# Kernel optimization log

Measured on AMD Instinct MI355X. Metric: run time of the kernel, lower is better.

Reference implementation:

```python
import jax, jax.numpy as jnp
import numpy as np

# fp4 e2m1 representable magnitudes and rounding midpoints
FP4_LEVELS = jnp.array([0.0, 0.5, 1.0, 1.5, 2.0, 3.0, 4.0, 6.0], dtype=jnp.float32)
FP4_BOUNDS = jnp.array([0.25, 0.75, 1.25, 1.75, 2.5, 3.5, 5.0], dtype=jnp.float32)
EPS = 1e-8
RANK = 64      # activation_lowrank_svd
NITER = 2      # activation_lowrank_niter


def fp4_get_scalar(x):
    # per-tensor scale: amax / max_fp4e2m1 (6.0)
    return jnp.maximum(jnp.max(jnp.abs(x)) / 6.0, EPS)


def fp4_qdq(x):
    # quant (round-to-nearest fp4e2m1 grid) followed by rquant (dequant)
    s = fp4_get_scalar(x)
    y = x / s
    a = jnp.clip(jnp.abs(y), 0.0, 6.0)
    idx = jnp.searchsorted(FP4_BOUNDS, a)  # nearest-level index
    return jnp.sign(y) * FP4_LEVELS[idx] * s


def power_iter_svd(G, V0, niter):
    # Dion-style power iteration: G ~ U diag(S) V^T, V0: [n,k]
    V = V0
    U = None
    W = None
    for it in range(niter):
        P = G @ V                                  # [m,k]
        U, _ = jnp.linalg.qr(P)                    # reduced QR, U: [m,k]
        W = G.T @ U                                # [n,k]
        if it < niter - 1:
            V = W / (jnp.linalg.norm(W, axis=0, keepdims=True) + EPS)
    S = jnp.linalg.norm(W, axis=0)                 # [k]
    Vn = W / (S[None, :] + EPS)                    # [n,k]
    return U, S, Vn


def svd_quant(x2d, V0):
    # low-rank kernel + fp4-quantized factors + fp4-quantized residual
    U, S, V = power_iter_svd(x2d, V0, NITER)
    ug = U.T                                       # [k,m]
    vg = V.T                                       # [k,n]
    ker = (U * S[None, :]) @ vg                    # [m,n] full-precision kernel
    ugq = fp4_qdq(ug)
    vgq = fp4_qdq(vg)
    res_q = fp4_qdq(x2d - ker)                     # quantized residual
    return (ugq.T * S[None, :]) @ vgq + res_q      # reconstructed input


def setup_inputs() -> dict:
    key = jax.random.key(0)
    k1, k2, k3, k4 = jax.random.split(key, 4)
    B, Sq, Din, Dout, R = 4, 2048, 4096, 4096, RANK
    x = jax.random.normal(k1, (B, Sq, Din), jnp.float32)
    weight = jax.random.normal(k2, (Dout, Din), jnp.float32) * (1.0 / np.sqrt(Din))
    bias = jax.random.normal(k3, (Dout,), jnp.float32) * 0.01
    V0 = jax.random.normal(k4, (Din, R), jnp.float32)  # cached subspace (state)
    return {"x": x, "weight": weight, "bias": bias, "V0": V0}


def reference(x, weight, bias, V0):
    B, Sq, Din = x.shape
    # activation SVD + fp4 quantization on flattened [B*S, Din]
    xq = svd_quant(x.reshape(-1, Din), V0).reshape(B, Sq, Din)
    # weight fp4 quant/dequant
    wq = fp4_qdq(weight)
    return xq @ wq.T + bias
```

## Files before the change

### kernel.cpp

```cpp
#include <hip/hip_runtime.h>
#include <stdint.h>

#define EPSF 1e-8f
#define KT 4160

typedef float  f32x4  __attribute__((ext_vector_type(4)));
typedef __bf16 bf16x8 __attribute__((ext_vector_type(8)));
typedef __bf16 bf16x4 __attribute__((ext_vector_type(4)));

constexpr size_t oP    = 0;
constexpr size_t oW    = oP  + 8192*64;
constexpr size_t oG    = oW  + 4096*64;
constexpr size_t oM1   = oG  + 64*64;
constexpr size_t oScal = oM1 + 64*4096;
constexpr size_t nZero1= oScal + 4;
constexpr size_t nZero2= oG + 64*64;
constexpr size_t oS    = nZero1;
constexpr size_t oLinv = oS + 64;
constexpr size_t oV    = oLinv + 64*64;
constexpr size_t oU    = oV + 4096*64;
constexpr size_t endF32= oU + 8192*64;
constexpr size_t bfByte= ((endF32*4 + 255)/256)*256;
constexpr size_t oVq   = 0;
constexpr size_t oA    = oVq + 64*4096;
constexpr size_t oB    = oA + (size_t)8192*4160;
constexpr size_t oVcT  = oB + (size_t)4096*4160;
constexpr size_t oUT   = oVcT + 3*(size_t)64*4096;
constexpr size_t oUhl  = oUT + 3*(size_t)64*8192;
constexpr size_t oKVT  = oUhl + 2*(size_t)8192*64;
constexpr size_t endBF = oKVT + 2*(size_t)4096*64;
constexpr size_t WS_NEED = bfByte + endBF*2;

__device__ __forceinline__ float qlevel(float a){
  if (a <= 0.25f) return 0.0f;
  if (a <= 0.75f) return 0.5f;
  if (a <= 1.25f) return 1.0f;
  if (a <= 1.75f) return 1.5f;
  if (a <= 2.5f)  return 2.0f;
  if (a <= 3.5f)  return 3.0f;
  if (a <= 5.0f)  return 4.0f;
  return 6.0f;
}
__device__ __forceinline__ float qgrid(float v, float s){
  float y = v / s;
  float l = qlevel(fabsf(y));
  return y < 0.0f ? -l : l;
}

__global__ void k_zero(float* p, int n){
  for (int i = blockIdx.x*blockDim.x + threadIdx.x; i < n; i += gridDim.x*blockDim.x)
    p[i] = 0.0f;
}

__global__ void k_amax4(const float4* __restrict__ x, int n4, unsigned* __restrict__ out){
  float m = 0.f;
  for (int i = blockIdx.x*blockDim.x + threadIdx.x; i < n4; i += gridDim.x*blockDim.x){
    float4 v = x[i];
    m = fmaxf(m, fmaxf(fmaxf(fabsf(v.x), fabsf(v.y)), fmaxf(fabsf(v.z), fabsf(v.w))));
  }
  for (int o = 32; o > 0; o >>= 1) m = fmaxf(m, __shfl_down(m, o, 64));
  __shared__ float sm[4];
  int lane = threadIdx.x & 63, w = threadIdx.x >> 6;
  if (lane == 0) sm[w] = m;
  __syncthreads();
  if (threadIdx.x == 0)
    atomicMax(out, __float_as_uint(fmaxf(fmaxf(sm[0],sm[1]), fmaxf(sm[2],sm[3]))));
}

__global__ __launch_bounds__(256) void k_gv(
    float* __restrict__ P, const float* __restrict__ x,
    const __bf16* __restrict__ Bh, const __bf16* __restrict__ Bm, const __bf16* __restrict__ Bl){
  int m0 = blockIdx.x * 128;
  int d0 = blockIdx.y * 512;
  int lane = threadIdx.x & 63, wave = threadIdx.x >> 6;
  int kgrp = lane >> 4, lrow = lane & 15;
  f32x4 acc[2][4] = {};
  for (int dc = d0; dc < d0 + 512; dc += 32){
    bf16x8 ah[2], am[2], al[2];
    #pragma unroll
    for (int f = 0; f < 2; f++){
      const float* g = x + (size_t)(m0 + wave*32 + f*16 + lrow)*4096 + dc + kgrp*8;
      float4 a = *(const float4*)g;
      float4 b = *(const float4*)(g + 4);
      float v[8] = {a.x,a.y,a.z,a.w,b.x,b.y,b.z,b.w};
      #pragma unroll
      for (int j = 0; j < 8; j++){
        __bf16 h = (__bf16)v[j];
        float r1 = v[j] - (float)h;
        __bf16 md = (__bf16)r1;
        float r2 = r1 - (float)md;
        ah[f][j] = h; am[f][j] = md; al[f][j] = (__bf16)r2;
      }
    }
    #pragma unroll
    for (int n = 0; n < 4; n++){
      size_t bo = (size_t)(n*16 + lrow)*4096 + dc + kgrp*8;
      bf16x8 bh = *(const bf16x8*)(Bh + bo);
      bf16x8 bm = *(const bf16x8*)(Bm + bo);
      bf16x8 bl = *(const bf16x8*)(Bl + bo);
      #pragma unroll
      for (int f = 0; f < 2; f++){
        acc[f][n] = __builtin_amdgcn_mfma_f32_16x16x32_bf16(ah[f], bh, acc[f][n],0,0,0);
        acc[f][n] = __builtin_amdgcn_mfma_f32_16x16x32_bf16(ah[f], bm, acc[f][n],0,0,0);
        acc[f][n] = __builtin_amdgcn_mfma_f32_16x16x32_bf16(am[f], bh, acc[f][n],0,0,0);
        acc[f][n] = __builtin_amdgcn_mfma_f32_16x16x32_bf16(ah[f], bl, acc[f][n],0,0,0);
        acc[f][n] = __builtin_amdgcn_mfma_f32_16x16x32_bf16(al[f], bh, acc[f][n],0,0,0);
        acc[f][n] = __builtin_amdgcn_mfma_f32_16x16x32_bf16(am[f], bm, acc[f][n],0,0,0);
      }
    }
  }
  #pragma unroll
  for (int f = 0; f < 2; f++)
    #pragma unroll
    for (int n = 0; n < 4; n++)
      #pragma unroll
      for (int r = 0; r < 4; r++)
        atomicAdd(&P[(size_t)(m0 + wave*32 + f*16 + kgrp*4 + r)*64 + n*16 + lrow], acc[f][n][r]);
}

__global__ __launch_bounds__(256) void k_gtu(
    float* __restrict__ W, const float* __restrict__ x,
    const __bf16* __restrict__ Bh, const __bf16* __restrict__ Bm, const __bf16* __restrict__ Bl){
  int d0 = blockIdx.x * 64;
  int m0 = blockIdx.y * 1024;
  int lane = threadIdx.x & 63, wave = threadIdx.x >> 6;
  int kgrp = lane >> 4, lrow = lane & 15;
  int dcol = d0 + wave*16 + lrow;
  f32x4 acc[4] = {};
  for (int mc = m0; mc < m0 + 1024; mc += 32){
    bf16x8 ah, am, al;
    int mb = mc + kgrp*8;
    #pragma unroll
    for (int j = 0; j < 8; j++){
      float v = x[(size_t)(mb + j)*4096 + dcol];
      __bf16 h = (__bf16)v;
      float r1 = v - (float)h;
      __bf16 md = (__bf16)r1;
      float r2 = r1 - (float)md;
      ah[j] = h; am[j] = md; al[j] = (__bf16)r2;
    }
    #pragma unroll
    for (int n = 0; n < 4; n++){
      size_t bo = (size_t)(n*16 + lrow)*8192 + mc + kgrp*8;
      bf16x8 bh = *(const bf16x8*)(Bh + bo);
      bf16x8 bm = *(const bf16x8*)(Bm + bo);
      bf16x8 bl = *(const bf16x8*)(Bl + bo);
      acc[n] = __builtin_amdgcn_mfma_f32_16x16x32_bf16(ah, bh, acc[n],0,0,0);
      acc[n] = __builtin_amdgcn_mfma_f32_16x16x32_bf16(ah, bm, acc[n],0,0,0);
      acc[n] = __builtin_amdgcn_mfma_f32_16x16x32_bf16(am, bh, acc[n],0,0,0);
      acc[n] = __builtin_amdgcn_mfma_f32_16x16x32_bf16(ah, bl, acc[n],0,0,0);
      acc[n] = __builtin_amdgcn_mfma_f32_16x16x32_bf16(al, bh, acc[n],0,0,0);
      acc[n] = __builtin_amdgcn_mfma_f32_16x16x32_bf16(am, bm, acc[n],0,0,0);
    }
  }
  #pragma unroll
  for (int n = 0; n < 4; n++)
    #pragma unroll
    for (int r = 0; r < 4; r++)
      atomicAdd(&W[(size_t)(d0 + wave*16 + kgrp*4 + r)*64 + n*16 + lrow], acc[n][r]);
}

__global__ void k_gram(const float* __restrict__ P, float* __restrict__ Gram){
  __shared__ float Pt[128][65];
  int m0 = blockIdx.x * 128;
  int t = threadIdx.x;
  for (int i = 0; i < 32; i++){
    int idx = i*256 + t; int r = idx >> 6, c = idx & 63;
    Pt[r][c] = P[(size_t)(m0+r)*64 + c];
  }
  __syncthreads();
  int ti = t >> 4, tj = t & 15;
  float acc[4][4] = {};
  for (int r = 0; r < 128; r++){
    float a[4], b[4];
    #pragma unroll
    for (int q = 0; q < 4; q++) a[q] = Pt[r][ti*4+q];
    #pragma unroll
    for (int q = 0; q < 4; q++) b[q] = Pt[r][tj*4+q];
    #pragma unroll
    for (int xx = 0; xx < 4; xx++)
      #pragma unroll
      for (int y = 0; y < 4; y++) acc[xx][y] += a[xx]*b[y];
  }
  for (int xx = 0; xx < 4; xx++)
    for (int y = 0; y < 4; y++)
      atomicAdd(&Gram[(ti*4+xx)*64 + tj*4+y], acc[xx][y]);
}

__global__ void k_cholinv(const float* __restrict__ Gram, float* __restrict__ Linv){
  __shared__ double A[64][64];
  __shared__ double Li[64][64];
  int t = threadIdx.x;
  for (int j = 0; j < 64; j++){ A[t][j] = (double)Gram[t*64+j]; Li[t][j] = 0.0; }
  __syncthreads();
  for (int k = 0; k < 64; k++){
    if (t == k) A[k][k] = sqrt(A[k][k]);
    __syncthreads();
    if (t > k) A[t][k] /= A[k][k];
    __syncthreads();
    if (t > k){
      double aik = A[t][k];
      for (int j = k+1; j <= t; j++) A[t][j] -= aik * A[j][k];
    }
    __syncthreads();
  }
  for (int i = t; i < 64; i++){
    double s = (i == t) ? 1.0 : 0.0;
    for (int p = t; p < i; p++) s -= A[i][p] * Li[p][t];
    Li[i][t] = s / A[i][i];
  }
  __syncthreads();
  for (int j = 0; j < 64; j++) Linv[t*64+j] = (float)Li[t][j];
}

__global__ void k_applyq(float* __restrict__ U, const float* __restrict__ P,
                         const float* __restrict__ Linv){
  __shared__ float Pt[64][65];
  __shared__ float Lt[64][65];
  int m0 = blockIdx.x * 64;
  int t = threadIdx.x;
  for (int i = 0; i < 16; i++){
    int idx = i*256 + t; int r = idx >> 6, c = idx & 63;
    Pt[r][c] = P[(size_t)(m0+r)*64 + c];
    Lt[r][c] = Linv[r*64 + c];
  }
  __syncthreads();
  int tm = t >> 4, tj = t & 15;
  float acc[4][4] = {};
  for (int i = 0; i < 64; i++){
    float p[4], lv[4];
    #pragma unroll
    for (int a = 0; a < 4; a++) p[a]  = Pt[tm*4+a][i];
    #pragma unroll
    for (int b = 0; b < 4; b++) lv[b] = Lt[tj*4+b][i];
    #pragma unroll
    for (int a = 0; a < 4; a++)
      #pragma unroll
      for (int b = 0; b < 4; b++) acc[a][b] += p[a]*lv[b];
  }
  for (int a = 0; a < 4; a++)
    for (int b = 0; b < 4; b++)
      U[(size_t)(m0+tm*4+a)*64 + tj*4+b] = acc[a][b];
}

__global__ void k_colnorm(const float* __restrict__ W, float* __restrict__ cn){
  int k = blockIdx.x;
  float s = 0.f;
  for (int d = threadIdx.x; d < 4096; d += 256){
    float v = W[(size_t)d*64 + k];
    s += v*v;
  }
  for (int o = 32; o > 0; o >>= 1) s += __shfl_down(s, o, 64);
  __shared__ float sm[4];
  int lane = threadIdx.x & 63, w = threadIdx.x >> 6;
  if (lane == 0) sm[w] = s;
  __syncthreads();
  if (threadIdx.x == 0) cn[k] = sqrtf(sm[0]+sm[1]+sm[2]+sm[3]);
}

__global__ void k_vnorm(float* __restrict__ V, const float* __restrict__ W,
                        const float* __restrict__ cn){
  int i = blockIdx.x*256 + threadIdx.x;
  int k = i & 63;
  V[i] = W[i] / (cn[k] + EPSF);
}

__global__ void k_vnkv(float* __restrict__ V, __bf16* __restrict__ Kh, __bf16* __restrict__ Kl,
                       const float* __restrict__ W, const float* __restrict__ S,
                       unsigned* __restrict__ amaxv){
  int i = blockIdx.x*256 + threadIdx.x;
  int k = i & 63, d = i >> 6;
  float s = S[k];
  float vn = W[i] / (s + EPSF);
  V[i] = vn;
  float kv = s * vn;
  __bf16 h = (__bf16)kv;
  Kh[(size_t)d*64 + k] = h;
  Kl[(size_t)d*64 + k] = (__bf16)(kv - (float)h);
  float m = fabsf(vn);
  for (int o = 32; o > 0; o >>= 1) m = fmaxf(m, __shfl_down(m, o, 64));
  __shared__ float sm[4];
  int lane = threadIdx.x & 63, w = threadIdx.x >> 6;
  if (lane == 0) sm[w] = m;
  __syncthreads();
  if (threadIdx.x == 0)
    atomicMax(amaxv, __float_as_uint(fmaxf(fmaxf(sm[0],sm[1]), fmaxf(sm[2],sm[3]))));
}

__global__ void k_prep_vct(const float* __restrict__ Vc, __bf16* __restrict__ Th,
                           __bf16* __restrict__ Tm, __bf16* __restrict__ Tl){
  __shared__ float Vt[64][65];
  int d0 = blockIdx.x * 64;
  int t = threadIdx.x;
  for (int i = 0; i < 16; i++){
    int idx = i*256 + t; int r = idx >> 6, c = idx & 63;
    Vt[r][c] = Vc[(size_t)(d0 + r)*64 + c];
  }
  __syncthreads();
  for (int i = 0; i < 16; i++){
    int idx = i*256 + t; int k = idx >> 6, dd = idx & 63;
    float v = Vt[dd][k];
    __bf16 h = (__bf16)v;
    float r1 = v - (float)h;
    __bf16 md = (__bf16)r1;
    float r2 = r1 - (float)md;
    size_t o = (size_t)k*4096 + d0 + dd;
    Th[o] = h; Tm[o] = md; Tl[o] = (__bf16)r2;
  }
}

__global__ void k_prep_u(const float* __restrict__ Ub, __bf16* __restrict__ Uh, __bf16* __restrict__ Ul,
                         __bf16* __restrict__ Th, __bf16* __restrict__ Tm, __bf16* __restrict__ Tl){
  __shared__ float Ut[64][65];
  int m0 = blockIdx.x * 64;
  int t = threadIdx.x;
  for (int i = 0; i < 16; i++){
    int idx = i*256 + t; int r = idx >> 6, c = idx & 63;
    float v = Ub[(size_t)(m0 + r)*64 + c];
    Ut[r][c] = v;
    __bf16 h = (__bf16)v;
    Uh[(size_t)(m0+r)*64 + c] = h;
    Ul[(size_t)(m0+r)*64 + c] = (__bf16)(v - (float)h);
  }
  __syncthreads();
  for (int i = 0; i < 16; i++){
    int idx = i*256 + t; int k = idx >> 6, mm = idx & 63;
    float v = Ut[mm][k];
    __bf16 h = (__bf16)v;
    float r1 = v - (float)h;
    __bf16 md = (__bf16)r1;
    float r2 = r1 - (float)md;
    size_t o = (size_t)k*8192 + m0 + mm;
    Th[o] = h; Tm[o] = md; Tl[o] = (__bf16)r2;
  }
}

__global__ void k_qw(__bf16* __restrict__ Bq, const float* __restrict__ w,
                     const unsigned* __restrict__ amaxw){
  float s = fmaxf(__uint_as_float(*amaxw) / 6.0f, EPSF);
  int i = blockIdx.x*256 + threadIdx.x;
  int n = i >> 10, d = (i & 1023)*4;
  float4 v = *(const float4*)(w + (size_t)n*4096 + d);
  bf16x4 o;
  o[0] = (__bf16)qgrid(v.x, s); o[1] = (__bf16)qgrid(v.y, s);
  o[2] = (__bf16)qgrid(v.z, s); o[3] = (__bf16)qgrid(v.w, s);
  *(bf16x4*)(Bq + (size_t)n*4160 + d) = o;
}

__global__ void k_qu(__bf16* __restrict__ Aq, const float* __restrict__ U,
                     const unsigned* __restrict__ amaxu){
  float s = fmaxf(__uint_as_float(*amaxu) / 6.0f, EPSF);
  int i = blockIdx.x*256 + threadIdx.x;
  int m = i >> 6, k = i & 63;
  Aq[(size_t)m*4160 + 4096 + k] = (__bf16)qgrid(U[i], s);
}

__global__ void k_qv(__bf16* __restrict__ Vq, const float* __restrict__ V,
                     const unsigned* __restrict__ amaxv){
  __shared__ float Vt[64][65];
  float s = fmaxf(__uint_as_float(*amaxv)/6.0f, EPSF);
  int d0 = blockIdx.x * 64;
  int t = threadIdx.x;
  for (int i = 0; i < 16; i++){
    int idx = i*256 + t; int r = idx >> 6, c = idx & 63;
    Vt[r][c] = V[(size_t)(d0 + r)*64 + c];
  }
  __syncthreads();
  for (int i = 0; i < 16; i++){
    int idx = i*256 + t; int k = idx >> 6, dd = idx & 63;
    Vq[(size_t)k*4096 + d0 + dd] = (__bf16)qgrid(Vt[dd][k], s);
  }
}

__global__ __launch_bounds__(256) void k_res(
    const float* __restrict__ x, const __bf16* __restrict__ Uh, const __bf16* __restrict__ Ul,
    const __bf16* __restrict__ Kh, const __bf16* __restrict__ Kl,
    unsigned* __restrict__ amaxr, __bf16* __restrict__ Aq, int mode){
  int m0 = blockIdx.x * 64, n0 = blockIdx.y * 128;
  int lane = threadIdx.x & 63, wave = threadIdx.x >> 6;
  int kgrp = lane >> 4, lrow = lane & 15;
  int mrow = m0 + wave*16 + lrow;
  f32x4 acc[8] = {};
  #pragma unroll
  for (int ks = 0; ks < 2; ks++){
    size_t ao = (size_t)mrow*64 + ks*32 + kgrp*8;
    bf16x8 uh = *(const bf16x8*)(Uh + ao);
    bf16x8 ul = *(const bf16x8*)(Ul + ao);
    #pragma unroll
    for (int n = 0; n < 8; n++){
      size_t bo = (size_t)(n0 + n*16 + lrow)*64 + ks*32 + kgrp*8;
      bf16x8 kh = *(const bf16x8*)(Kh + bo);
      bf16x8 kl = *(const bf16x8*)(Kl + bo);
      acc[n] = __builtin_amdgcn_mfma_f32_16x16x32_bf16(uh, kh, acc[n],0,0,0);
      acc[n] = __builtin_amdgcn_mfma_f32_16x16x32_bf16(uh, kl, acc[n],0,0,0);
      acc[n] = __builtin_amdgcn_mfma_f32_16x16x32_bf16(ul, kh, acc[n],0,0,0);
    }
  }
  int mb = m0 + wave*16 + kgrp*4;
  if (mode == 0){
    float mx = 0.f;
    #pragma unroll
    for (int n = 0; n < 8; n++){
      int c = n0 + n*16 + lrow;
      #pragma unroll
      for (int r = 0; r < 4; r++)
        mx = fmaxf(mx, fabsf(x[(size_t)(mb + r)*4096 + c] - acc[n][r]));
    }
    for (int o = 32; o > 0; o >>= 1) mx = fmaxf(mx, __shfl_down(mx, o, 64));
    __shared__ float sm[4];
    if (lane == 0) sm[wave] = mx;
    __syncthreads();
    if (threadIdx.x == 0)
      atomicMax(amaxr, __float_as_uint(fmaxf(fmaxf(sm[0],sm[1]), fmaxf(sm[2],sm[3]))));
  } else {
    float s = fmaxf(__uint_as_float(*amaxr)/6.0f, EPSF);
    #pragma unroll
    for (int n = 0; n < 8; n++){
      int c = n0 + n*16 + lrow;
      #pragma unroll
      for (int r = 0; r < 4; r++)
        Aq[(size_t)(mb + r)*4160 + c] =
          (__bf16)qgrid(x[(size_t)(mb + r)*4096 + c] - acc[n][r], s);
    }
  }
}

__global__ __launch_bounds__(256) void k_m1(
    float* __restrict__ M1g, const __bf16* __restrict__ Vq, const __bf16* __restrict__ Bq){
  int n0 = blockIdx.x * 64;
  int k0 = blockIdx.y * 512;
  int lane = threadIdx.x & 63, wave = threadIdx.x >> 6;
  int kgrp = lane >> 4, lrow = lane & 15;
  int nrow = n0 + wave*16 + lrow;
  f32x4 acc[4] = {};
  for (int kc = k0; kc < k0 + 512; kc += 32){
    bf16x8 fb = *(const bf16x8*)(Bq + (size_t)nrow*4160 + kc + kgrp*8);
    #pragma unroll
    for (int mt = 0; mt < 4; mt++){
      bf16x8 fa = *(const bf16x8*)(Vq + (size_t)(mt*16 + lrow)*4096 + kc + kgrp*8);
      acc[mt] = __builtin_amdgcn_mfma_f32_16x16x32_bf16(fa, fb, acc[mt],0,0,0);
    }
  }
  #pragma unroll
  for (int mt = 0; mt < 4; mt++)
    #pragma unroll
    for (int r = 0; r < 4; r++)
      atomicAdd(&M1g[(size_t)(mt*16 + kgrp*4 + r)*4096 + nrow], acc[mt][r]);
}

__global__ void k_m2t(__bf16* __restrict__ Bq, const float* __restrict__ M1g,
                      const float* __restrict__ S, const unsigned* __restrict__ scal){
  float su = fmaxf(__uint_as_float(scal[1])/6.0f, EPSF);
  float sv = fmaxf(__uint_as_float(scal[2])/6.0f, EPSF);
  float sr = fmaxf(__uint_as_float(scal[3])/6.0f, EPSF);
  int i = blockIdx.x*256 + threadIdx.x;
  int n = i >> 6, k = i & 63;
  float v = M1g[(size_t)k*4096 + n] * (su * sv * S[k] / sr);
  Bq[(size_t)n*4160 + 4096 + k] = (__bf16)v;
}

__global__ __launch_bounds__(256)
void k_gemm(float* __restrict__ out, const __bf16* __restrict__ A,
            const __bf16* __restrict__ B, const float* __restrict__ bias,
            const unsigned* __restrict__ scal){
  __shared__ __align__(16) __bf16 As[128*64];
  __shared__ __align__(16) __bf16 Bs[128*64];
  int m0 = blockIdx.y * 128, n0 = blockIdx.x * 128;
  int t = threadIdx.x;
  int lane = t & 63;
  int wave = t >> 6;
  int wrow = wave & 1, wcol = wave >> 1;
  f32x4 acc[4][4] = {};

  for (int kt = 0; kt < KT; kt += 64){
    #pragma unroll
    for (int i = 0; i < 4; i++){
      int idx = i*256 + t;
      int r = idx >> 3, slot = idx & 7;
      int c = slot ^ (r & 7);
      const __bf16* ga = A + (size_t)(m0 + r)*KT + kt + c*8;
      const __bf16* gb = B + (size_t)(n0 + r)*KT + kt + c*8;
      __bf16* la = As + (size_t)(i*256 + (t & ~63))*8;
      __bf16* lb = Bs + (size_t)(i*256 + (t & ~63))*8;
      __builtin_amdgcn_global_load_lds((const __attribute__((address_space(1))) uint32_t*)ga,
                                       (__attribute__((address_space(3))) uint32_t*)la, 16, 0, 0);
      __builtin_amdgcn_global_load_lds((const __attribute__((address_space(1))) uint32_t*)gb,
                                       (__attribute__((address_space(3))) uint32_t*)lb, 16, 0, 0);
    }
    __syncthreads();
    #pragma unroll
    for (int ks = 0; ks < 2; ks++){
      bf16x8 fa[4], fb[4];
      int c = ks*4 + (lane >> 4);
      #pragma unroll
      for (int f = 0; f < 4; f++){
        int row = wrow*64 + f*16 + (lane & 15);
        fa[f] = *(const bf16x8*)(As + ((size_t)row*8 + (c ^ (row & 7)))*8);
        int col = wcol*64 + f*16 + (lane & 15);
        fb[f] = *(const bf16x8*)(Bs + ((size_t)col*8 + (c ^ (col & 7)))*8);
      }
      #pragma unroll
      for (int fm = 0; fm < 4; fm++)
        #pragma unroll
        for (int fn = 0; fn < 4; fn++)
          acc[fm][fn] = __builtin_amdgcn_mfma_f32_16x16x32_bf16(fa[fm], fb[fn], acc[fm][fn], 0, 0, 0);
    }
    __syncthreads();
  }

  float sr = fmaxf(__uint_as_float(scal[3])/6.0f, EPSF);
  float sw = fmaxf(__uint_as_float(scal[0])/6.0f, EPSF);
  float srw = sr * sw;
  #pragma unroll
  for (int fn = 0; fn < 4; fn++){
    int n = n0 + wcol*64 + fn*16 + (lane & 15);
    float bs = bias[n];
    #pragma unroll
    for (int fm = 0; fm < 4; fm++){
      int mb = m0 + wrow*64 + fm*16 + 4*(lane >> 4);
      #pragma unroll
      for (int r = 0; r < 4; r++)
        out[(size_t)(mb + r)*4096 + n] = acc[fm][fn][r] * srw + bs;
    }
  }
}

extern "C" void kernel_launch(void* const* d_in, const int* in_sizes, int n_in,
                              void* d_out, int out_size, void* d_ws, size_t ws_size,
                              hipStream_t stream){
  const float* x    = (const float*)d_in[0];
  const float* wt   = (const float*)d_in[1];
  const float* bias = (const float*)d_in[2];
  const float* V0   = (const float*)d_in[3];
  float* out = (float*)d_out;
  if (ws_size < WS_NEED) return;

  float* F = (float*)d_ws;
  unsigned* scal = (unsigned*)(F + oScal);
  __bf16* BFp = (__bf16*)((char*)d_ws + bfByte);
  __bf16* Vq  = BFp + oVq;
  __bf16* Aq  = BFp + oA;
  __bf16* Bq  = BFp + oB;
  __bf16* VcTh = BFp + oVcT,              *VcTm = VcTh + (size_t)64*4096, *VcTl = VcTm + (size_t)64*4096;
  __bf16* UTh  = BFp + oUT,               *UTm  = UTh + (size_t)64*8192,  *UTl  = UTm + (size_t)64*8192;
  __bf16* Uh   = BFp + oUhl,              *Ul   = Uh + (size_t)8192*64;
  __bf16* KVTh = BFp + oKVT,              *KVTl = KVTh + (size_t)4096*64;
  float *P = F+oP, *W = F+oW, *Gm = F+oG, *M1 = F+oM1, *Sv = F+oS,
        *Li = F+oLinv, *V = F+oV, *Ub = F+oU;

  dim3 b256(256);
  k_zero <<<dim3(2048), b256, 0, stream>>>(F, (int)nZero1);
  k_amax4<<<dim3(1024), b256, 0, stream>>>((const float4*)wt, 4194304, scal+0);
  k_qw   <<<dim3(16384), b256, 0, stream>>>(Bq, wt, scal+0);

  k_prep_vct<<<dim3(64),  b256, 0, stream>>>(V0, VcTh, VcTm, VcTl);
  k_gv     <<<dim3(64,8), b256, 0, stream>>>(P, x, VcTh, VcTm, VcTl);
  k_gram   <<<dim3(64),   b256, 0, stream>>>(P, Gm);
  k_cholinv<<<dim3(1), dim3(64), 0, stream>>>(Gm, Li);
  k_applyq <<<dim3(128),  b256, 0, stream>>>(Ub, P, Li);
  k_prep_u <<<dim3(128),  b256, 0, stream>>>(Ub, Uh, Ul, UTh, UTm, UTl);
  k_gtu    <<<dim3(64,8), b256, 0, stream>>>(W, x, UTh, UTm, UTl);
  k_colnorm<<<dim3(64),   b256, 0, stream>>>(W, Sv);
  k_vnorm  <<<dim3(1024), b256, 0, stream>>>(V, W, Sv);

  k_prep_vct<<<dim3(64),  b256, 0, stream>>>(V, VcTh, VcTm, VcTl);
  k_zero   <<<dim3(2048), b256, 0, stream>>>(F, (int)nZero2);
  k_gv     <<<dim3(64,8), b256, 0, stream>>>(P, x, VcTh, VcTm, VcTl);
  k_gram   <<<dim3(64),   b256, 0, stream>>>(P, Gm);
  k_cholinv<<<dim3(1), dim3(64), 0, stream>>>(Gm, Li);
  k_applyq <<<dim3(128),  b256, 0, stream>>>(Ub, P, Li);
  k_prep_u <<<dim3(128),  b256, 0, stream>>>(Ub, Uh, Ul, UTh, UTm, UTl);
  k_gtu    <<<dim3(64,8), b256, 0, stream>>>(W, x, UTh, UTm, UTl);
  k_colnorm<<<dim3(64),   b256, 0, stream>>>(W, Sv);
  k_vnkv   <<<dim3(1024), b256, 0, stream>>>(V, KVTh, KVTl, W, Sv, scal+2);

  k_amax4<<<dim3(1024), b256, 0, stream>>>((const float4*)Ub, 131072, scal+1);
  k_qu   <<<dim3(2048), b256, 0, stream>>>(Aq, Ub, scal+1);
  k_qv   <<<dim3(64),   b256, 0, stream>>>(Vq, V, scal+2);
  k_res  <<<dim3(128,32), b256, 0, stream>>>(x, Uh, Ul, KVTh, KVTl, scal+3, Aq, 0);
  k_res  <<<dim3(128,32), b256, 0, stream>>>(x, Uh, Ul, KVTh, KVTl, scal+3, Aq, 1);

  k_m1  <<<dim3(64,8), b256, 0, stream>>>(M1, Vq, Bq);
  k_m2t <<<dim3(1024), b256, 0, stream>>>(Bq, M1, Sv, scal);
  k_gemm<<<dim3(32,64), b256, 0, stream>>>(out, Aq, Bq, bias, scal);
}
```

Baseline: 1.634 ms.

## Enlarge GEMM tiles to 256x256 with 4-stage async LDS pipeline

Reworks the final bf16 GEMM from 128x128 tiles with 256 threads and a synchronous load/compute loop into 256x256 tiles with 512 threads. A 4-deep ring of 32-wide K slices in LDS is filled by direct global-to-LDS loads issued three steps ahead, and partial vmcnt waits with a single barrier per step replace the two syncthreads. MFMA issue priority is raised with setprio. The aim is to hide global load latency and raise arithmetic intensity per block, at the cost of 128 KB of LDS, more accumulator registers, and fewer blocks (512).

```diff
diff --git a/kernel.cpp b/kernel.cpp
--- a/kernel.cpp
+++ b/kernel.cpp
@@ -459,68 +459,97 @@
   Bq[(size_t)n*4160 + 4096 + k] = (__bf16)v;
 }
 
-__global__ __launch_bounds__(256)
+__global__ __launch_bounds__(512, 2)
 void k_gemm(float* __restrict__ out, const __bf16* __restrict__ A,
             const __bf16* __restrict__ B, const float* __restrict__ bias,
             const unsigned* __restrict__ scal){
-  __shared__ __align__(16) __bf16 As[128*64];
-  __shared__ __align__(16) __bf16 Bs[128*64];
-  int m0 = blockIdx.y * 128, n0 = blockIdx.x * 128;
-  int t = threadIdx.x;
-  int lane = t & 63;
-  int wave = t >> 6;
-  int wrow = wave & 1, wcol = wave >> 1;
-  f32x4 acc[4][4] = {};
-
-  for (int kt = 0; kt < KT; kt += 64){
-    #pragma unroll
-    for (int i = 0; i < 4; i++){
-      int idx = i*256 + t;
-      int r = idx >> 3, slot = idx & 7;
-      int c = slot ^ (r & 7);
-      const __bf16* ga = A + (size_t)(m0 + r)*KT + kt + c*8;
-      const __bf16* gb = B + (size_t)(n0 + r)*KT + kt + c*8;
-      __bf16* la = As + (size_t)(i*256 + (t & ~63))*8;
-      __bf16* lb = Bs + (size_t)(i*256 + (t & ~63))*8;
+  __shared__ __align__(16) __bf16 As[4*8192];
+  __shared__ __align__(16) __bf16 Bs[4*8192];
+  const int m0 = blockIdx.y * 256, n0 = blockIdx.x * 256;
+  const int tid = threadIdx.x;
+  const int lane = tid & 63, wave = tid >> 6;
+  const int wrow = wave >> 2, wcol = wave & 3;
+  const int kg = lane >> 4, lr = lane & 15;
+  f32x4 acc[8][4] = {};
+
+  auto STAGE = [&](int tt){
+    __bf16* as = &As[(tt & 3) * 8192];
+    __bf16* bs = &Bs[(tt & 3) * 8192];
+    const int kt = tt * 32;
+    #pragma unroll
+    for (int q = 0; q < 2; q++){
+      int idx = q * 512 + tid;
+      int rp  = idx >> 3;
+      int sp  = (idx & 7) ^ (rp & 7);
+      int grow = rp * 2 + (sp >> 2);
+      int gcol = (sp & 3) * 8;
+      const __bf16* ga = A + (size_t)(m0 + grow) * KT + kt + gcol;
+      const __bf16* gb = B + (size_t)(n0 + grow) * KT + kt + gcol;
+      __bf16* la = as + (size_t)(idx & ~63) * 8;
+      __bf16* lb = bs + (size_t)(idx & ~63) * 8;
       __builtin_amdgcn_global_load_lds((const __attribute__((address_space(1))) uint32_t*)ga,
                                        (__attribute__((address_space(3))) uint32_t*)la, 16, 0, 0);
       __builtin_amdgcn_global_load_lds((const __attribute__((address_space(1))) uint32_t*)gb,
                                        (__attribute__((address_space(3))) uint32_t*)lb, 16, 0, 0);
     }
-    __syncthreads();
-    #pragma unroll
-    for (int ks = 0; ks < 2; ks++){
-      bf16x8 fa[4], fb[4];
-      int c = ks*4 + (lane >> 4);
-      #pragma unroll
-      for (int f = 0; f < 4; f++){
-        int row = wrow*64 + f*16 + (lane & 15);
-        fa[f] = *(const bf16x8*)(As + ((size_t)row*8 + (c ^ (row & 7)))*8);
-        int col = wcol*64 + f*16 + (lane & 15);
-        fb[f] = *(const bf16x8*)(Bs + ((size_t)col*8 + (c ^ (col & 7)))*8);
-      }
-      #pragma unroll
-      for (int fm = 0; fm < 4; fm++)
-        #pragma unroll
-        for (int fn = 0; fn < 4; fn++)
-          acc[fm][fn] = __builtin_amdgcn_mfma_f32_16x16x32_bf16(fa[fm], fb[fn], acc[fm][fn], 0, 0, 0);
-    }
-    __syncthreads();
-  }
+  };
+
+  auto BODY = [&](int t, bool stage){
+    const __bf16* as = &As[(t & 3) * 8192];
+    const __bf16* bs = &Bs[(t & 3) * 8192];
+    bf16x8 fa[8], fb[4];
+    #pragma unroll
+    for (int mf = 0; mf < 8; mf++){
+      int row = wrow*128 + mf*16 + lr;
+      int rp  = row >> 1;
+      int sl  = (((row & 1) << 2) | kg) ^ (rp & 7);
+      fa[mf] = *(const bf16x8*)(as + (size_t)rp*64 + sl*8);
+    }
+    #pragma unroll
+    for (int nf = 0; nf < 4; nf++){
+      int row = wcol*64 + nf*16 + lr;
+      int rp  = row >> 1;
+      int sl  = (((row & 1) << 2) | kg) ^ (rp & 7);
+      fb[nf] = *(const bf16x8*)(bs + (size_t)rp*64 + sl*8);
+    }
+    if (stage) STAGE(t + 3);
+    __builtin_amdgcn_s_setprio(1);
+    #pragma unroll
+    for (int mf = 0; mf < 8; mf++)
+      #pragma unroll
+      for (int nf = 0; nf < 4; nf++)
+        acc[mf][nf] = __builtin_amdgcn_mfma_f32_16x16x32_bf16(fa[mf], fb[nf], acc[mf][nf], 0, 0, 0);
+    __builtin_amdgcn_s_setprio(0);
+  };
+
+  STAGE(0); STAGE(1); STAGE(2);
+
+  const int NT = KT / 32;
+  for (int t = 0; t < NT - 2; t++){
+    asm volatile("s_waitcnt vmcnt(8)" ::: "memory");
+    __builtin_amdgcn_s_barrier();
+    BODY(t, t < NT - 3);
+  }
+  asm volatile("s_waitcnt vmcnt(4)" ::: "memory");
+  __builtin_amdgcn_s_barrier();
+  BODY(NT - 2, false);
+  asm volatile("s_waitcnt vmcnt(0)" ::: "memory");
+  __builtin_amdgcn_s_barrier();
+  BODY(NT - 1, false);
 
   float sr = fmaxf(__uint_as_float(scal[3])/6.0f, EPSF);
   float sw = fmaxf(__uint_as_float(scal[0])/6.0f, EPSF);
   float srw = sr * sw;
   #pragma unroll
-  for (int fn = 0; fn < 4; fn++){
-    int n = n0 + wcol*64 + fn*16 + (lane & 15);
-    float bs = bias[n];
-    #pragma unroll
-    for (int fm = 0; fm < 4; fm++){
-      int mb = m0 + wrow*64 + fm*16 + 4*(lane >> 4);
+  for (int nf = 0; nf < 4; nf++){
+    int n = n0 + wcol*64 + nf*16 + lr;
+    float bv = bias[n];
+    #pragma unroll
+    for (int mf = 0; mf < 8; mf++){
+      int mb = m0 + wrow*128 + mf*16 + 4*kg;
       #pragma unroll
       for (int r = 0; r < 4; r++)
-        out[(size_t)(mb + r)*4096 + n] = acc[fm][fn][r] * srw + bs;
+        out[(size_t)(mb + r)*4096 + n] = acc[mf][nf][r]*srw + bv;
     }
   }
 }
@@ -582,5 +611,5 @@
 
   k_m1  <<<dim3(64,8), b256, 0, stream>>>(M1, Vq, Bq);
   k_m2t <<<dim3(1024), b256, 0, stream>>>(Bq, M1, Sv, scal);
-  k_gemm<<<dim3(32,64), b256, 0, stream>>>(out, Aq, Bq, bias, scal);
-}
+  k_gemm<<<dim3(16,32), dim3(512), 0, stream>>>(out, Aq, Bq, bias, scal);
+}
```

Measured after the change: 1.515 ms. -7.3%, faster.
